# Performance work log

Hardware: AMD Instinct MI355X
Metric: run time of the kernel (lower is better)

The kernel has to match this reference:

```python
import jax, jax.numpy as jnp
import numpy as np

B, L, D2, C = 64, 512, 512, 50  # D2 = hidden_size*2

def setup_inputs() -> dict:
    key = jax.random.key(0)
    ks = jax.random.split(key, 8)
    text_vec = jax.random.normal(ks[0], (B, L, D2), dtype=jnp.float32)
    text_mask = jnp.ones((B, L), dtype=bool)
    sbj_bound = jnp.sort(jax.random.randint(ks[1], (B, 2), 0, L), axis=-1)
    obj_start = jax.random.randint(ks[2], (B, L), 0, C)
    obj_end = jax.random.randint(ks[3], (B, L), 0, C)
    W_start = jax.random.normal(ks[4], (2 * D2, C), dtype=jnp.float32) * 0.02
    b_start = jnp.zeros((C,), dtype=jnp.float32)
    W_end = jax.random.normal(ks[5], (2 * D2, C), dtype=jnp.float32) * 0.02
    b_end = jnp.zeros((C,), dtype=jnp.float32)
    return {"text_vec": text_vec, "text_mask": text_mask, "sbj_bound": sbj_bound,
            "obj_start": obj_start, "obj_end": obj_end,
            "W_start": W_start, "b_start": b_start, "W_end": W_end, "b_end": b_end}

def _masked_ce(logits, labels, maskf, value_num):
    # logits [B,L,C], labels [B,L]
    logp = jax.nn.log_softmax(logits, axis=-1)
    nll = -jnp.take_along_axis(logp, labels[..., None], axis=-1)[..., 0]
    return (nll * maskf).sum() / value_num

def reference(text_vec, text_mask, sbj_bound, obj_start, obj_end,
              W_start, b_start, W_end, b_end):
    pos = jnp.arange(L)  # [L]
    start, end = sbj_bound[:, 0], sbj_bound[:, 1]
    # inclusive span mask, vectorized replacement for the per-example loop
    span = ((pos[None, :] >= start[:, None]) & (pos[None, :] <= end[:, None])).astype(text_vec.dtype)  # [B,L]
    count = span.sum(axis=1, keepdims=True)  # [B,1], >=1 since start<=end
    sbj_vec = jnp.einsum('bl,bld->bd', span, text_vec) / count  # segment mean [B,D2]
    # cat([text_vec, sbj_vec]) @ W  ==  text_vec @ W[:D2] + sbj_vec @ W[D2:]
    def head(W, b):
        return (jnp.einsum('bld,dc->blc', text_vec, W[:D2])
                + (sbj_vec @ W[D2:])[:, None, :] + b)
    o1 = head(W_start, b_start)
    o2 = head(W_end, b_end)
    maskf = text_mask.astype(jnp.float32)
    value_num = maskf.sum()
    loss_obj_s = _masked_ce(o1, obj_start, maskf, value_num)
    loss_obj_e = _masked_ce(o2, obj_end, maskf, value_num)
    return loss_obj_s + loss_obj_e
```

## Files before the change

kernel.cpp:

```cpp
#include <hip/hip_runtime.h>
#include <math.h>

#define BB 64
#define LL 512
#define DD 512
#define CC 50
#define NC 100
#define NCP 112
#define WST 520

#define WSB_LOSS  0
#define WSB_CNT   4
#define WSB_DONE  8
#define WSB_SCOMB 64
#define WSB_PART  28736
#define WSB_WTOP  553024
#define WSB_WBOT  667712

typedef __attribute__((ext_vector_type(8))) short bf16x8;
typedef __attribute__((ext_vector_type(4))) float f32x4;

static __device__ __forceinline__ unsigned short f2bf(float x) {
    unsigned int u = __float_as_uint(x);
    u += 0x7FFFu + ((u >> 16) & 1u);
    return (unsigned short)(u >> 16);
}
static __device__ __forceinline__ float bf2f(unsigned short h) {
    return __uint_as_float(((unsigned int)h) << 16);
}

__global__ __launch_bounds__(256) void k_prep(
    const float* __restrict__ tv, const int* __restrict__ sbj_bound,
    const float* __restrict__ Wst, const float* __restrict__ Wen,
    char* __restrict__ wsb)
{
    __shared__ float sh[128 * 53];
    const int t = threadIdx.x;
    const int blk = blockIdx.x;

    if (blk < 512) {
        const int b = blk >> 3, seg = blk & 7;
        const int start = sbj_bound[2 * b], end = sbj_bound[2 * b + 1];
        int r0 = seg * 64;      if (r0 < start) r0 = start;
        int r1 = seg * 64 + 63; if (r1 > end)   r1 = end;
        const int c4 = t & 127, par = t >> 7;
        const float* bp = tv + (size_t)b * LL * DD + c4 * 4;
        float4 a0 = {0, 0, 0, 0}, a1 = {0, 0, 0, 0};
        int r = r0 + par;
        for (; r + 2 <= r1; r += 4) {
            float4 v0 = *(const float4*)(bp + (size_t)r * DD);
            float4 v1 = *(const float4*)(bp + (size_t)(r + 2) * DD);
            a0.x += v0.x; a0.y += v0.y; a0.z += v0.z; a0.w += v0.w;
            a1.x += v1.x; a1.y += v1.y; a1.z += v1.z; a1.w += v1.w;
        }
        for (; r <= r1; r += 2) {
            float4 v0 = *(const float4*)(bp + (size_t)r * DD);
            a0.x += v0.x; a0.y += v0.y; a0.z += v0.z; a0.w += v0.w;
        }
        float4* buf = (float4*)sh;
        float4 acc = {a0.x + a1.x, a0.y + a1.y, a0.z + a1.z, a0.w + a1.w};
        buf[t] = acc;
        __syncthreads();
        if (t < 128) {
            float4 x = buf[t], y = buf[t + 128];
            unsigned short* part = (unsigned short*)(wsb + WSB_PART);
            ushort4 o;
            o.x = f2bf(x.x + y.x); o.y = f2bf(x.y + y.y);
            o.z = f2bf(x.z + y.z); o.w = f2bf(x.w + y.w);
            *(ushort4*)(part + ((size_t)(seg * BB + b)) * DD + t * 4) = o;
        }
    } else {
        const int bi = blk - 512;
        const int mat = bi >> 3;
        const int cj = bi & 7;
        const float* W = mat ? Wen : Wst;
        const int kbase = cj * 128;
        const float* src = W + (size_t)kbase * CC;
#pragma unroll
        for (int i = 0; i < 25; i++) {
            int idx = t + i * 256;
            int kr = idx / 50, c = idx - kr * 50;
            sh[kr * 53 + c] = src[idx];
        }
        __syncthreads();
        unsigned short* outp =
            (unsigned short*)(wsb + ((cj < 4) ? WSB_WTOP : WSB_WBOT));
        const int kout = kbase & 511;
#pragma unroll
        for (int i = 0; i < 25; i++) {
            int idx = t + i * 256;
            int n = idx >> 7, kl = idx & 127;
            outp[((size_t)(mat * CC + n)) * DD + kout + kl] = f2bf(sh[kl * 53 + n]);
        }
        if (bi == 0 && t == 0) {
            *(float*)(wsb + WSB_LOSS) = 0.0f;
            *(float*)(wsb + WSB_CNT)  = 0.0f;
            *(int*)(wsb + WSB_DONE)   = 0;
        }
    }
}

__global__ __launch_bounds__(256) void k_scomb(
    const int* __restrict__ sbj_bound,
    const float* __restrict__ bst, const float* __restrict__ ben,
    char* __restrict__ wsb)
{
    __shared__ __align__(16) unsigned short sbjb[16 * WST];
    const int t = threadIdx.x;
    const int g = blockIdx.x;
    const unsigned short* part = (const unsigned short*)(wsb + WSB_PART);

#pragma unroll
    for (int i = 0; i < 8; i++) {
        int idx = t + i * 256;
        int bo = idx >> 7, d4 = idx & 127;
        int b = g * 16 + bo;
        float inv = 1.0f / (float)(sbj_bound[2 * b + 1] - sbj_bound[2 * b] + 1);
        float sx = 0.f, sy = 0.f, sz = 0.f, sw = 0.f;
#pragma unroll
        for (int seg = 0; seg < 8; seg++) {
            ushort4 v = *(const ushort4*)(part + ((size_t)(seg * BB + b)) * DD + d4 * 4);
            sx += bf2f(v.x); sy += bf2f(v.y); sz += bf2f(v.z); sw += bf2f(v.w);
        }
        ushort4 o;
        o.x = f2bf(sx * inv); o.y = f2bf(sy * inv);
        o.z = f2bf(sz * inv); o.w = f2bf(sw * inv);
        *(ushort4*)(sbjb + bo * WST + d4 * 4) = o;
    }
    __syncthreads();

    const int wv = t >> 6, ln = t & 63, tc = ln & 15, quad = ln >> 4;
    const unsigned short* wbot = (const unsigned short*)(wsb + WSB_WBOT);
    float* scomb = (float*)(wsb + WSB_SCOMB);
    const unsigned short* Af = sbjb + tc * WST + quad * 8;
    const int nu = (wv < 3) ? 2 : 1;
    for (int j = 0; j < nu; j++) {
        const int u = wv * 2 + j;
        f32x4 acc = (f32x4)(0.0f);
        const unsigned short* Bf = wbot + (size_t)(u * 16 + tc) * DD + quad * 8;
#pragma unroll
        for (int kk = 0; kk < DD; kk += 32) {
            bf16x8 af = *(const bf16x8*)(Af + kk);
            bf16x8 bf = *(const bf16x8*)(Bf + kk);
            acc = __builtin_amdgcn_mfma_f32_16x16x32_bf16(af, bf, acc, 0, 0, 0);
        }
        const int cc = u * 16 + tc;
        const float bias = (cc < CC) ? bst[cc] : ((cc < NC) ? ben[cc - CC] : 0.0f);
#pragma unroll
        for (int i = 0; i < 4; i++) {
            int b = g * 16 + quad * 4 + i;
            scomb[b * NCP + cc] = acc[i] + bias;
        }
    }
}

__global__ __launch_bounds__(512, 2) void k_main(
    const float* __restrict__ tv,
    const int* __restrict__ mask,
    const int* __restrict__ obj_s, const int* __restrict__ obj_e,
    char* __restrict__ wsb, float* __restrict__ out)
{
    __shared__ __align__(16) unsigned short Wt[NCP * WST];
    __shared__ float red[16];
    const int t = threadIdx.x, wv = t >> 6, ln = t & 63;
    const int tc = ln & 15, quad = ln >> 4;
    const int m0w = blockIdx.x * 128 + wv * 16;
    const int b = blockIdx.x >> 2;
    const unsigned short* wtop = (const unsigned short*)(wsb + WSB_WTOP);

    const float* Abase = tv + (size_t)(m0w + tc) * DD + quad * 8;

    float4 alo[16];
#pragma unroll
    for (int j = 0; j < 8; j++) {
        alo[2 * j]     = *(const float4*)(Abase + j * 32);
        alo[2 * j + 1] = *(const float4*)(Abase + j * 32 + 4);
    }
#pragma unroll
    for (int i = 0; i < 14; i++) {
        int idx = t + i * 512;
        int n = idx >> 6, ch = idx & 63;
        *(bf16x8*)(Wt + n * WST + ch * 8) =
            *(const bf16x8*)(wtop + (size_t)n * DD + ch * 8);
    }
    float4 ahi[16];
#pragma unroll
    for (int j = 0; j < 8; j++) {
        ahi[2 * j]     = *(const float4*)(Abase + 256 + j * 32);
        ahi[2 * j + 1] = *(const float4*)(Abase + 256 + j * 32 + 4);
    }
    __syncthreads();

    f32x4 acc[7];
#pragma unroll
    for (int u = 0; u < 7; u++) acc[u] = (f32x4)(0.0f);
    const unsigned short* Wf = Wt + tc * WST + quad * 8;

#pragma unroll
    for (int j = 0; j < 8; j++) {
        float4 v0 = alo[2 * j], v1 = alo[2 * j + 1];
        bf16x8 af;
        af[0] = (short)f2bf(v0.x); af[1] = (short)f2bf(v0.y);
        af[2] = (short)f2bf(v0.z); af[3] = (short)f2bf(v0.w);
        af[4] = (short)f2bf(v1.x); af[5] = (short)f2bf(v1.y);
        af[6] = (short)f2bf(v1.z); af[7] = (short)f2bf(v1.w);
#pragma unroll
        for (int u = 0; u < 7; u++) {
            bf16x8 bf = *(const bf16x8*)(Wf + u * 16 * WST + j * 32);
            acc[u] = __builtin_amdgcn_mfma_f32_16x16x32_bf16(af, bf, acc[u], 0, 0, 0);
        }
    }
#pragma unroll
    for (int j = 0; j < 8; j++) {
        float4 v0 = ahi[2 * j], v1 = ahi[2 * j + 1];
        bf16x8 af;
        af[0] = (short)f2bf(v0.x); af[1] = (short)f2bf(v0.y);
        af[2] = (short)f2bf(v0.z); af[3] = (short)f2bf(v0.w);
        af[4] = (short)f2bf(v1.x); af[5] = (short)f2bf(v1.y);
        af[6] = (short)f2bf(v1.z); af[7] = (short)f2bf(v1.w);
#pragma unroll
        for (int u = 0; u < 7; u++) {
            bf16x8 bf = *(const bf16x8*)(Wf + u * 16 * WST + 256 + j * 32);
            acc[u] = __builtin_amdgcn_mfma_f32_16x16x32_bf16(af, bf, acc[u], 0, 0, 0);
        }
    }

    const float* scomb = (const float*)(wsb + WSB_SCOMB);
    float sc[7];
#pragma unroll
    for (int u = 0; u < 7; u++) sc[u] = scomb[b * NCP + u * 16 + tc];

    float loss_local = 0.0f, cnt_local = 0.0f;
#pragma unroll
    for (int i = 0; i < 4; i++) {
        const int l = (m0w + quad * 4 + i) & (LL - 1);
        const int lab1 = obj_s[b * LL + l];
        const int lab2 = obj_e[b * LL + l] + CC;
        const int mk   = mask[b * LL + l];
        float lg[7];
#pragma unroll
        for (int u = 0; u < 7; u++) lg[u] = acc[u][i] + sc[u];
        float m1 = fmaxf(fmaxf(lg[0], lg[1]), lg[2]);
        if (tc < 2) m1 = fmaxf(m1, lg[3]);
        float m2 = fmaxf(lg[4], lg[5]);
        if (tc >= 2) m2 = fmaxf(m2, lg[3]);
        if (tc < 4)  m2 = fmaxf(m2, lg[6]);
#pragma unroll
        for (int off = 1; off < 16; off <<= 1) {
            m1 = fmaxf(m1, __shfl_xor(m1, off, 16));
            m2 = fmaxf(m2, __shfl_xor(m2, off, 16));
        }
        float e1 = expf(lg[0] - m1) + expf(lg[1] - m1) + expf(lg[2] - m1)
                 + ((tc < 2) ? expf(lg[3] - m1) : 0.0f);
        float e2 = expf(lg[4] - m2) + expf(lg[5] - m2)
                 + ((tc >= 2) ? expf(lg[3] - m2) : 0.0f)
                 + ((tc < 4)  ? expf(lg[6] - m2) : 0.0f);
        float t1 = 0.0f, t2 = 0.0f;
#pragma unroll
        for (int u = 0; u < 7; u++) {
            const int cc = u * 16 + tc;
            if (cc == lab1) t1 = lg[u];
            if (cc == lab2) t2 = lg[u];
        }
#pragma unroll
        for (int off = 1; off < 16; off <<= 1) {
            e1 += __shfl_xor(e1, off, 16);
            e2 += __shfl_xor(e2, off, 16);
            t1 += __shfl_xor(t1, off, 16);
            t2 += __shfl_xor(t2, off, 16);
        }
        if (tc == 0) {
            const float nll = (m1 + logf(e1) - t1) + (m2 + logf(e2) - t2);
            loss_local += mk ? nll : 0.0f;
            cnt_local  += mk ? 1.0f : 0.0f;
        }
    }
#pragma unroll
    for (int off = 1; off < 64; off <<= 1) {
        loss_local += __shfl_xor(loss_local, off);
        cnt_local  += __shfl_xor(cnt_local, off);
    }
    if (ln == 0) { red[wv * 2] = loss_local; red[wv * 2 + 1] = cnt_local; }
    __syncthreads();
    if (t == 0) {
        float Ls = 0.f, Cs = 0.f;
#pragma unroll
        for (int w = 0; w < 8; w++) { Ls += red[w * 2]; Cs += red[w * 2 + 1]; }
        float* wsf = (float*)wsb;
        atomicAdd(&wsf[0], Ls);
        atomicAdd(&wsf[1], Cs);
        __threadfence();
        int old = atomicAdd((int*)(wsb + WSB_DONE), 1);
        if (old == (int)gridDim.x - 1) {
            float L = atomicAdd(&wsf[0], 0.0f);
            float C = atomicAdd(&wsf[1], 0.0f);
            out[0] = L / C;
        }
    }
}

extern "C" void kernel_launch(void* const* d_in, const int* in_sizes, int n_in,
                              void* d_out, int out_size, void* d_ws, size_t ws_size,
                              hipStream_t stream) {
    const float* tv   = (const float*)d_in[0];
    const int*   mask = (const int*)d_in[1];
    const int*   sbj  = (const int*)d_in[2];
    const int*   objs = (const int*)d_in[3];
    const int*   obje = (const int*)d_in[4];
    const float* Wst  = (const float*)d_in[5];
    const float* bst  = (const float*)d_in[6];
    const float* Wen  = (const float*)d_in[7];
    const float* ben  = (const float*)d_in[8];
    float* out = (float*)d_out;
    char*  wsb = (char*)d_ws;

    k_prep<<<528, 256, 0, stream>>>(tv, sbj, Wst, Wen, wsb);
    k_scomb<<<4, 256, 0, stream>>>(sbj, bst, ben, wsb);
    k_main<<<256, 512, 0, stream>>>(tv, mask, objs, obje, wsb, out);
}
```

Before: 138.1 us.

## Pre-convert A to bf16 registers, hoist label/scomb loads, widen scomb block

k_main now converts the fp32 text rows to bf16 fragments before the barrier, and loads the scomb bias, labels and mask ahead of the MFMA loop. This takes conversion and global-load latency off the critical path after the shared-memory W load. The occupancy hint drops from 2 blocks to 1 so the larger register footprint fits. k_scomb moves to 512 threads so each of 7 waves computes one 16-column tile, which shortens that small serial kernel.

```diff
diff --git a/kernel.cpp b/kernel.cpp
--- a/kernel.cpp
+++ b/kernel.cpp
@@ -100,7 +100,7 @@
     }
 }
 
-__global__ __launch_bounds__(256) void k_scomb(
+__global__ __launch_bounds__(512) void k_scomb(
     const int* __restrict__ sbj_bound,
     const float* __restrict__ bst, const float* __restrict__ ben,
     char* __restrict__ wsb)
@@ -111,8 +111,8 @@
     const unsigned short* part = (const unsigned short*)(wsb + WSB_PART);
 
 #pragma unroll
-    for (int i = 0; i < 8; i++) {
-        int idx = t + i * 256;
+    for (int i = 0; i < 4; i++) {
+        int idx = t + i * 512;
         int bo = idx >> 7, d4 = idx & 127;
         int b = g * 16 + bo;
         float inv = 1.0f / (float)(sbj_bound[2 * b + 1] - sbj_bound[2 * b] + 1);
@@ -130,12 +130,11 @@
     __syncthreads();
 
     const int wv = t >> 6, ln = t & 63, tc = ln & 15, quad = ln >> 4;
-    const unsigned short* wbot = (const unsigned short*)(wsb + WSB_WBOT);
-    float* scomb = (float*)(wsb + WSB_SCOMB);
-    const unsigned short* Af = sbjb + tc * WST + quad * 8;
-    const int nu = (wv < 3) ? 2 : 1;
-    for (int j = 0; j < nu; j++) {
-        const int u = wv * 2 + j;
+    if (wv < 7) {
+        const unsigned short* wbot = (const unsigned short*)(wsb + WSB_WBOT);
+        float* scomb = (float*)(wsb + WSB_SCOMB);
+        const unsigned short* Af = sbjb + tc * WST + quad * 8;
+        const int u = wv;
         f32x4 acc = (f32x4)(0.0f);
         const unsigned short* Bf = wbot + (size_t)(u * 16 + tc) * DD + quad * 8;
 #pragma unroll
@@ -154,7 +153,7 @@
     }
 }
 
-__global__ __launch_bounds__(512, 2) void k_main(
+__global__ __launch_bounds__(512, 1) void k_main(
     const float* __restrict__ tv,
     const int* __restrict__ mask,
     const int* __restrict__ obj_s, const int* __restrict__ obj_e,
@@ -170,24 +169,57 @@
 
     const float* Abase = tv + (size_t)(m0w + tc) * DD + quad * 8;
 
-    float4 alo[16];
-#pragma unroll
-    for (int j = 0; j < 8; j++) {
-        alo[2 * j]     = *(const float4*)(Abase + j * 32);
-        alo[2 * j + 1] = *(const float4*)(Abase + j * 32 + 4);
-    }
-#pragma unroll
-    for (int i = 0; i < 14; i++) {
-        int idx = t + i * 512;
-        int n = idx >> 6, ch = idx & 63;
-        *(bf16x8*)(Wt + n * WST + ch * 8) =
-            *(const bf16x8*)(wtop + (size_t)n * DD + ch * 8);
-    }
-    float4 ahi[16];
-#pragma unroll
-    for (int j = 0; j < 8; j++) {
-        ahi[2 * j]     = *(const float4*)(Abase + 256 + j * 32);
-        ahi[2 * j + 1] = *(const float4*)(Abase + 256 + j * 32 + 4);
+    bf16x8 areg[16];
+    {
+        float4 t0[8], t1[8];
+#pragma unroll
+        for (int j = 0; j < 8; j++) {
+            t0[j] = *(const float4*)(Abase + j * 32);
+            t1[j] = *(const float4*)(Abase + j * 32 + 4);
+        }
+#pragma unroll
+        for (int i = 0; i < 14; i++) {
+            int idx = t + i * 512;
+            int n = idx >> 6, ch = idx & 63;
+            *(bf16x8*)(Wt + n * WST + ch * 8) =
+                *(const bf16x8*)(wtop + (size_t)n * DD + ch * 8);
+        }
+#pragma unroll
+        for (int j = 0; j < 8; j++) {
+            bf16x8 af;
+            af[0] = (short)f2bf(t0[j].x); af[1] = (short)f2bf(t0[j].y);
+            af[2] = (short)f2bf(t0[j].z); af[3] = (short)f2bf(t0[j].w);
+            af[4] = (short)f2bf(t1[j].x); af[5] = (short)f2bf(t1[j].y);
+            af[6] = (short)f2bf(t1[j].z); af[7] = (short)f2bf(t1[j].w);
+            areg[j] = af;
+        }
+#pragma unroll
+        for (int j = 0; j < 8; j++) {
+            t0[j] = *(const float4*)(Abase + 256 + j * 32);
+            t1[j] = *(const float4*)(Abase + 256 + j * 32 + 4);
+        }
+#pragma unroll
+        for (int j = 0; j < 8; j++) {
+            bf16x8 af;
+            af[0] = (short)f2bf(t0[j].x); af[1] = (short)f2bf(t0[j].y);
+            af[2] = (short)f2bf(t0[j].z); af[3] = (short)f2bf(t0[j].w);
+            af[4] = (short)f2bf(t1[j].x); af[5] = (short)f2bf(t1[j].y);
+            af[6] = (short)f2bf(t1[j].z); af[7] = (short)f2bf(t1[j].w);
+            areg[8 + j] = af;
+        }
+    }
+
+    const float* scomb = (const float*)(wsb + WSB_SCOMB);
+    float sc[7];
+#pragma unroll
+    for (int u = 0; u < 7; u++) sc[u] = scomb[b * NCP + u * 16 + tc];
+    int lab1[4], lab2[4], mk[4];
+#pragma unroll
+    for (int i = 0; i < 4; i++) {
+        const int l = (m0w + quad * 4 + i) & (LL - 1);
+        lab1[i] = obj_s[b * LL + l];
+        lab2[i] = obj_e[b * LL + l] + CC;
+        mk[i]   = mask[b * LL + l];
     }
     __syncthreads();
 
@@ -197,46 +229,18 @@
     const unsigned short* Wf = Wt + tc * WST + quad * 8;
 
 #pragma unroll
-    for (int j = 0; j < 8; j++) {
-        float4 v0 = alo[2 * j], v1 = alo[2 * j + 1];
-        bf16x8 af;
-        af[0] = (short)f2bf(v0.x); af[1] = (short)f2bf(v0.y);
-        af[2] = (short)f2bf(v0.z); af[3] = (short)f2bf(v0.w);
-        af[4] = (short)f2bf(v1.x); af[5] = (short)f2bf(v1.y);
-        af[6] = (short)f2bf(v1.z); af[7] = (short)f2bf(v1.w);
+    for (int j = 0; j < 16; j++) {
+        bf16x8 af = areg[j];
 #pragma unroll
         for (int u = 0; u < 7; u++) {
             bf16x8 bf = *(const bf16x8*)(Wf + u * 16 * WST + j * 32);
             acc[u] = __builtin_amdgcn_mfma_f32_16x16x32_bf16(af, bf, acc[u], 0, 0, 0);
         }
     }
-#pragma unroll
-    for (int j = 0; j < 8; j++) {
-        float4 v0 = ahi[2 * j], v1 = ahi[2 * j + 1];
-        bf16x8 af;
-        af[0] = (short)f2bf(v0.x); af[1] = (short)f2bf(v0.y);
-        af[2] = (short)f2bf(v0.z); af[3] = (short)f2bf(v0.w);
-        af[4] = (short)f2bf(v1.x); af[5] = (short)f2bf(v1.y);
-        af[6] = (short)f2bf(v1.z); af[7] = (short)f2bf(v1.w);
-#pragma unroll
-        for (int u = 0; u < 7; u++) {
-            bf16x8 bf = *(const bf16x8*)(Wf + u * 16 * WST + 256 + j * 32);
-            acc[u] = __builtin_amdgcn_mfma_f32_16x16x32_bf16(af, bf, acc[u], 0, 0, 0);
-        }
-    }
-
-    const float* scomb = (const float*)(wsb + WSB_SCOMB);
-    float sc[7];
-#pragma unroll
-    for (int u = 0; u < 7; u++) sc[u] = scomb[b * NCP + u * 16 + tc];
 
     float loss_local = 0.0f, cnt_local = 0.0f;
 #pragma unroll
     for (int i = 0; i < 4; i++) {
-        const int l = (m0w + quad * 4 + i) & (LL - 1);
-        const int lab1 = obj_s[b * LL + l];
-        const int lab2 = obj_e[b * LL + l] + CC;
-        const int mk   = mask[b * LL + l];
         float lg[7];
 #pragma unroll
         for (int u = 0; u < 7; u++) lg[u] = acc[u][i] + sc[u];
@@ -259,8 +263,8 @@
 #pragma unroll
         for (int u = 0; u < 7; u++) {
             const int cc = u * 16 + tc;
-            if (cc == lab1) t1 = lg[u];
-            if (cc == lab2) t2 = lg[u];
+            if (cc == lab1[i]) t1 = lg[u];
+            if (cc == lab2[i]) t2 = lg[u];
         }
 #pragma unroll
         for (int off = 1; off < 16; off <<= 1) {
@@ -271,8 +275,8 @@
         }
         if (tc == 0) {
             const float nll = (m1 + logf(e1) - t1) + (m2 + logf(e2) - t2);
-            loss_local += mk ? nll : 0.0f;
-            cnt_local  += mk ? 1.0f : 0.0f;
+            loss_local += mk[i] ? nll : 0.0f;
+            cnt_local  += mk[i] ? 1.0f : 0.0f;
         }
     }
 #pragma unroll
@@ -315,6 +319,6 @@
     char*  wsb = (char*)d_ws;
 
     k_prep<<<528, 256, 0, stream>>>(tv, sbj, Wst, Wen, wsb);
-    k_scomb<<<4, 256, 0, stream>>>(sbj, bst, ben, wsb);
+    k_scomb<<<4, 512, 0, stream>>>(sbj, bst, ben, wsb);
     k_main<<<256, 512, 0, stream>>>(tv, mask, objs, obje, wsb, out);
 }
```

New measurement: 140.2 us. About the same (+1.6%).
